# Kernel tuning notes

Hardware: AMD Instinct MI355X
Metric: run time of the kernel (lower is better)

## Reference

```python
import jax, jax.numpy as jnp
import numpy as np

N_NODES = 100000
N_EDGES = 800000
N_IN = 256
N_H = 128


def setup_inputs() -> dict:
    key = jax.random.key(0)
    ks = jax.random.split(key, 8)
    x_1 = jax.random.normal(ks[0], (1, N_NODES, N_IN), dtype=jnp.float32)
    x_2 = jax.random.normal(ks[1], (1, N_NODES, N_IN), dtype=jnp.float32)
    edge_index = jax.random.randint(ks[2], (2, N_EDGES), 0, N_NODES, dtype=jnp.int32)
    edge_weight = jax.random.uniform(ks[3], (N_EDGES,), dtype=jnp.float32)
    # xavier-uniform-ish init for fc weight (stored as [in, out])
    lim = float(np.sqrt(6.0 / (N_IN + N_H)))
    W_gcn = jax.random.uniform(ks[4], (N_IN, N_H), minval=-lim, maxval=lim, dtype=jnp.float32)
    gcn_bias = jnp.zeros((N_H,), dtype=jnp.float32)
    prelu_a = jnp.full((1,), 0.25, dtype=jnp.float32)  # PReLU default slope
    lim2 = float(np.sqrt(1.0 / N_H))
    lin_W = jax.random.uniform(ks[5], (N_H, N_H), minval=-lim2, maxval=lim2, dtype=jnp.float32)
    lin_b = jax.random.uniform(ks[6], (N_H,), minval=-lim2, maxval=lim2, dtype=jnp.float32)
    return {
        "x_1": x_1, "x_2": x_2, "edge_index": edge_index, "edge_weight": edge_weight,
        "W_gcn": W_gcn, "gcn_bias": gcn_bias, "prelu_a": prelu_a,
        "lin_W": lin_W, "lin_b": lin_b,
    }


def _prelu(x, a):
    return jnp.where(x >= 0, x, a * x)


def _gcn(feat, edge_index, edge_weight, W, b, a, n_nodes):
    # feat: [1, N, n_in] -> h: [N, n_h]
    h = jnp.squeeze(feat, 0) @ W
    row, col = edge_index[0], edge_index[1]
    # spmm: out[i] = sum_{e: row_e = i} w_e * h[col_e]
    msg = edge_weight[:, None] * h[col]            # [E, n_h]
    agg = jax.ops.segment_sum(msg, row, num_segments=n_nodes)  # [N, n_h]
    return _prelu(agg + b, a)                      # [N, n_h]


def reference(x_1, x_2, edge_index, edge_weight, W_gcn, gcn_bias, prelu_a, lin_W, lin_b):
    n = x_1.shape[1]
    h_1 = _gcn(x_1, edge_index, edge_weight, W_gcn, gcn_bias, prelu_a, n)
    h_2 = _gcn(x_2, edge_index, edge_weight, W_gcn, gcn_bias, prelu_a, n)
    z_1 = (h_1 @ lin_W + lin_b).sum(1)   # [N]
    z_2 = (h_2 @ lin_W + lin_b).sum(1)   # [N]
    return jnp.concatenate((z_1, z_2), 0)  # [2N]
```

## Files before the change

kernel.cpp:

```cpp
#include <hip/hip_runtime.h>

#define N_NODES 100000
#define N_EDGES 800000
#define N_IN    256
#define N_H     128
#define M_TOT   (2 * N_NODES)

typedef __bf16 bfx8 __attribute__((ext_vector_type(8)));
typedef unsigned short u16x8 __attribute__((ext_vector_type(8)));
typedef float fx4 __attribute__((ext_vector_type(4)));

__device__ inline unsigned short f2bf(float f) {
    union { float f; unsigned u; } v; v.f = f;
    return (unsigned short)((v.u + 0x7FFF + ((v.u >> 16) & 1)) >> 16);
}
__device__ inline float bf2f(unsigned short s) {
    union { unsigned u; float f; } v; v.u = ((unsigned)s) << 16;
    return v.f;
}

__device__ inline void async16(const void* g, void* l) {
    __builtin_amdgcn_global_load_lds((const __attribute__((address_space(1))) void*)g,
                                     (__attribute__((address_space(3))) void*)l, 16, 0, 0);
}

#define NSB2  3125
__global__ __launch_bounds__(256) void scatter_kernel(
        const int* __restrict__ ei, const float* __restrict__ ew,
        int* __restrict__ cursor, int2* __restrict__ edata) {
    int e = blockIdx.x * 256 + threadIdx.x;
    int row = ei[e];
    int pos = atomicAdd(cursor + row, 1);
    edata[pos] = make_int2(ei[N_EDGES + e] << 8, __float_as_int(ew[e]));
}

#define NT    12500
#define NTB1  6250
#define NGB3  1024

__global__ __launch_bounds__(256, 4) void gemm_kernel(
        const float* __restrict__ x1, const float* __restrict__ x2,
        const unsigned short* __restrict__ wT,
        unsigned short* __restrict__ hb) {
    __shared__ __align__(16) float Abuf[2][16][256];
    const int t = threadIdx.x;
    const int wv = t >> 6, ln = t & 63;
    const int quad = ln >> 4, l16 = ln & 15, sw = l16 & 7;

#define STAGE(buf, TT) do {                                                    \
        int br_ = (TT) >= NTB1;                                                \
        const float* xs_ = br_ ? x2 : x1;                                      \
        const float* base_ = xs_ + (size_t)((TT) - br_ * NTB1) * (16 * N_IN);  \
        _Pragma("unroll")                                                      \
        for (int i_ = 0; i_ < 4; ++i_) {                                       \
            int r_ = wv * 4 + i_;                                              \
            async16(base_ + (size_t)r_ * N_IN + ((ln ^ (r_ & 7)) << 2),        \
                    &Abuf[(buf)][r_][0]);                                      \
        }                                                                      \
    } while (0)

    int T = blockIdx.x;
    STAGE(0, T);

    bfx8 Bf[2][8];
#pragma unroll
    for (int c2 = 0; c2 < 2; ++c2)
#pragma unroll
        for (int kc = 0; kc < 8; ++kc)
            Bf[c2][kc] = *(const bfx8*)(wT +
                (size_t)(wv * 32 + c2 * 16 + l16) * N_IN + kc * 32 + quad * 8);
#pragma unroll
    for (int c2 = 0; c2 < 2; ++c2)
#pragma unroll
        for (int kc = 0; kc < 8; ++kc)
            asm volatile("" : "+v"(Bf[c2][kc]));

    int cur = 0;
    for (; T < NT; T += NGB3) {
        int Tn = T + NGB3;
        if (Tn < NT) {
            STAGE(cur ^ 1, Tn);
            asm volatile("s_waitcnt vmcnt(4)" ::: "memory");
        } else {
            asm volatile("s_waitcnt vmcnt(0)" ::: "memory");
        }
        asm volatile("s_barrier" ::: "memory");
        {
            int br = T >= NTB1;
            int node0 = (T - br * NTB1) * 16;
            fx4 acc0 = {0.f, 0.f, 0.f, 0.f}, acc1 = {0.f, 0.f, 0.f, 0.f};
            const float* rowp = &Abuf[cur][l16][0];
#pragma unroll
            for (int kc = 0; kc < 8; ++kc) {
                int s0 = kc * 8 + quad * 2;
                fx4 lo = *(const fx4*)(rowp + (((s0    ) ^ sw) << 2));
                fx4 hi = *(const fx4*)(rowp + (((s0 + 1) ^ sw) << 2));
                bfx8 af;
                af[0] = (__bf16)lo[0]; af[1] = (__bf16)lo[1];
                af[2] = (__bf16)lo[2]; af[3] = (__bf16)lo[3];
                af[4] = (__bf16)hi[0]; af[5] = (__bf16)hi[1];
                af[6] = (__bf16)hi[2]; af[7] = (__bf16)hi[3];
                acc0 = __builtin_amdgcn_mfma_f32_16x16x32_bf16(af, Bf[0][kc], acc0, 0, 0, 0);
                acc1 = __builtin_amdgcn_mfma_f32_16x16x32_bf16(af, Bf[1][kc], acc1, 0, 0, 0);
            }
            unsigned short* hp = hb + (size_t)node0 * 256 + br * 128 + wv * 32 + l16;
#pragma unroll
            for (int r = 0; r < 4; ++r) {
                size_t off = (size_t)(quad * 4 + r) * 256;
                hp[off]      = __builtin_bit_cast(unsigned short, (__bf16)acc0[r]);
                hp[off + 16] = __builtin_bit_cast(unsigned short, (__bf16)acc1[r]);
            }
        }
        asm volatile("s_barrier" ::: "memory");
        cur ^= 1;
    }
#undef STAGE
}

#define HIST_BLKS 3125
__global__ __launch_bounds__(256) void prep_kernel(const int* __restrict__ ei,
                                                   int* __restrict__ deg,
                                                   const float* __restrict__ W,
                                                   unsigned short* __restrict__ wT,
                                                   const float* __restrict__ linW,
                                                   const float* __restrict__ linb,
                                                   float* __restrict__ wsum) {
    const int t = threadIdx.x;
    if (blockIdx.x < HIST_BLKS) {
        int e = blockIdx.x * 256 + t;
        if (e < N_EDGES) atomicAdd(deg + ei[e], 1);
    } else if (blockIdx.x < HIST_BLKS + 32) {
        int kb = (blockIdx.x - HIST_BLKS) * 8;
#pragma unroll
        for (int p = 0; p < 4; ++p) {
            int idx = p * 256 + t;
            int k = kb + (idx >> 7), n = idx & 127;
            wT[(size_t)n * N_IN + k] = f2bf(W[(size_t)k * N_H + n]);
        }
    } else {
        int j = t;
        if (j < N_H) {
            float s = 0.f;
            for (int o = 0; o < N_H; ++o) s += linW[j * N_H + o];
            wsum[j] = s;
        }
        if (j == N_H) {
            float s = 0.f;
            for (int o = 0; o < N_H; ++o) s += linb[o];
            wsum[N_H] = s;
        }
    }
}

__global__ __launch_bounds__(256) void scan1_kernel(const int* __restrict__ deg,
                                                    int* __restrict__ part,
                                                    int* __restrict__ bsum) {
    __shared__ int s[256];
    int g = blockIdx.x * 256 + threadIdx.x;
    int v = (g < N_NODES) ? deg[g] : 0;
    s[threadIdx.x] = v;
    __syncthreads();
#pragma unroll
    for (int off = 1; off < 256; off <<= 1) {
        int t = (threadIdx.x >= off) ? s[threadIdx.x - off] : 0;
        __syncthreads();
        s[threadIdx.x] += t;
        __syncthreads();
    }
    if (g < N_NODES) part[g] = s[threadIdx.x] - v;
    if (threadIdx.x == 255) bsum[blockIdx.x] = s[255];
}

#define NBLK_SCAN 391
__global__ void scan2_kernel(int* __restrict__ bsum) {
    __shared__ int s[512];
    int v = (threadIdx.x < NBLK_SCAN) ? bsum[threadIdx.x] : 0;
    s[threadIdx.x] = v;
    __syncthreads();
#pragma unroll
    for (int off = 1; off < 512; off <<= 1) {
        int t = (threadIdx.x >= off) ? s[threadIdx.x - off] : 0;
        __syncthreads();
        s[threadIdx.x] += t;
        __syncthreads();
    }
    if (threadIdx.x < NBLK_SCAN) bsum[threadIdx.x] = s[threadIdx.x] - v;
}

__global__ __launch_bounds__(256) void scan3_kernel(const int* __restrict__ part,
                                                    const int* __restrict__ bsum,
                                                    int* __restrict__ off,
                                                    int* __restrict__ cursor) {
    int g = blockIdx.x * 256 + threadIdx.x;
    if (g < N_NODES) {
        int o = part[g] + bsum[blockIdx.x];
        off[g] = o;
        cursor[g] = o;
    }
    if (g == 0) off[N_NODES] = N_EDGES;
}

__global__ __launch_bounds__(256) void gcn_seg_kernel(const int* __restrict__ off,
                                                      const int2* __restrict__ edata,
                                                      const unsigned short* __restrict__ hb,
                                                      const float* __restrict__ gcn_bias,
                                                      const float* __restrict__ prelu_a,
                                                      const float* __restrict__ wsum,
                                                      float* __restrict__ zout) {
    const int wave = threadIdx.x >> 6, lane = threadIdx.x & 63;
    const int node = blockIdx.x * 4 + wave;
    const int s = __builtin_amdgcn_readfirstlane(off[node]);
    const int e = __builtin_amdgcn_readfirstlane(off[node + 1]);
    const int l2 = lane * 2;
    float a0 = 0.f, a1 = 0.f;
    float b0 = 0.f, b1 = 0.f;
    int i = s;
    for (; i + 1 < e; i += 2) {
        int2 E0 = edata[i], E1 = edata[i + 1];
        float w0 = __int_as_float(E0.y), w1 = __int_as_float(E1.y);
        ushort2 p10 = *(const ushort2*)(hb + E0.x + l2);
        ushort2 p20 = *(const ushort2*)(hb + E0.x + 128 + l2);
        ushort2 p11 = *(const ushort2*)(hb + E1.x + l2);
        ushort2 p21 = *(const ushort2*)(hb + E1.x + 128 + l2);
        a0 += w0 * bf2f(p10.x) + w1 * bf2f(p11.x);
        a1 += w0 * bf2f(p10.y) + w1 * bf2f(p11.y);
        b0 += w0 * bf2f(p20.x) + w1 * bf2f(p21.x);
        b1 += w0 * bf2f(p20.y) + w1 * bf2f(p21.y);
    }
    if (i < e) {
        int2 E0 = edata[i];
        float w0 = __int_as_float(E0.y);
        ushort2 p10 = *(const ushort2*)(hb + E0.x + l2);
        ushort2 p20 = *(const ushort2*)(hb + E0.x + 128 + l2);
        a0 += w0 * bf2f(p10.x);
        a1 += w0 * bf2f(p10.y);
        b0 += w0 * bf2f(p20.x);
        b1 += w0 * bf2f(p20.y);
    }
    const float alpha = prelu_a[0];
    const float g0 = gcn_bias[l2], g1 = gcn_bias[l2 + 1];
    const float q0 = wsum[l2],     q1 = wsum[l2 + 1];
    float v0 = a0 + g0, v1 = a1 + g1;
    float u0 = b0 + g0, u1 = b1 + g1;
    v0 = (v0 >= 0.f) ? v0 : alpha * v0;
    v1 = (v1 >= 0.f) ? v1 : alpha * v1;
    u0 = (u0 >= 0.f) ? u0 : alpha * u0;
    u1 = (u1 >= 0.f) ? u1 : alpha * u1;
    float s1 = v0 * q0 + v1 * q1;
    float s2 = u0 * q0 + u1 * q1;
#pragma unroll
    for (int o = 32; o; o >>= 1) {
        s1 += __shfl_down(s1, o, 64);
        s2 += __shfl_down(s2, o, 64);
    }
    if (lane == 0) {
        zout[node]           = s1 + wsum[128];
        zout[node + N_NODES] = s2 + wsum[128];
    }
}

extern "C" void kernel_launch(void* const* d_in, const int* in_sizes, int n_in,
                              void* d_out, int out_size, void* d_ws, size_t ws_size,
                              hipStream_t stream) {
    const float* x1 = (const float*)d_in[0];
    const float* x2 = (const float*)d_in[1];
    const int*   ei = (const int*)d_in[2];
    const float* ew = (const float*)d_in[3];
    const float* Wg = (const float*)d_in[4];
    const float* gb = (const float*)d_in[5];
    const float* pa = (const float*)d_in[6];
    const float* lW = (const float*)d_in[7];
    const float* lb = (const float*)d_in[8];
    float* zout = (float*)d_out;

    unsigned short* hb   = (unsigned short*)d_ws;
    int2*  edata  = (int2*)(hb + (size_t)M_TOT * N_H);
    unsigned short* wT   = (unsigned short*)(edata + N_EDGES);
    int*   deg    = (int*)(wT + N_IN * N_H);
    int*   part   = deg + 100096;
    int*   off    = part + 100096;
    int*   cursor = off + 100096;
    int*   bsum   = cursor + 100096;
    float* wsum   = (float*)(bsum + 512);

    hipMemsetAsync(deg, 0, (size_t)N_NODES * sizeof(int), stream);
    prep_kernel<<<HIST_BLKS + 33, 256, 0, stream>>>(ei, deg, Wg, wT, lW, lb, wsum);
    scan1_kernel<<<NBLK_SCAN, 256, 0, stream>>>(deg, part, bsum);
    scan2_kernel<<<1, 512, 0, stream>>>(bsum);
    scan3_kernel<<<NBLK_SCAN, 256, 0, stream>>>(part, bsum, off, cursor);
    scatter_kernel<<<NSB2, 256, 0, stream>>>(ei, ew, cursor, edata);
    gemm_kernel<<<NGB3, 256, 0, stream>>>(x1, x2, wT, hb);
    gcn_seg_kernel<<<N_NODES / 4, 256, 0, stream>>>(off, edata, hb, gb, pa, wsum, zout);
}
```

Baseline: 393.0 us.

## Fuse edge scatter into GEMM launch, drop persistent loop, unroll gather by four

Scatter and GEMM are merged into one launch: the first blocks do the edge scatter and the rest each compute one 16-row tile, replacing the persistent double-buffered GEMM loop. This removes a kernel boundary and lets the scatter overlap the GEMM. The lin_W row-sum in prep is reworked as a parallel wave reduction instead of a serial per-thread loop, and the gather loop in gcn_seg is unrolled to four edges per iteration for more loads in flight. The trade-off is that each GEMM block now reloads the B fragments and loses cross-tile prefetch overlap, with many more short-lived blocks.

```diff
diff --git a/kernel.cpp b/kernel.cpp
--- a/kernel.cpp
+++ b/kernel.cpp
@@ -24,43 +24,38 @@
                                      (__attribute__((address_space(3))) void*)l, 16, 0, 0);
 }
 
-#define NSB2  3125
-__global__ __launch_bounds__(256) void scatter_kernel(
+#define NTB1  6250
+#define NSB   3125
+#define NGB   12500
+
+__global__ __launch_bounds__(256, 4) void gemm_scatter_kernel(
+        const float* __restrict__ x1, const float* __restrict__ x2,
+        const unsigned short* __restrict__ wT,
+        unsigned short* __restrict__ hb,
         const int* __restrict__ ei, const float* __restrict__ ew,
         int* __restrict__ cursor, int2* __restrict__ edata) {
-    int e = blockIdx.x * 256 + threadIdx.x;
-    int row = ei[e];
-    int pos = atomicAdd(cursor + row, 1);
-    edata[pos] = make_int2(ei[N_EDGES + e] << 8, __float_as_int(ew[e]));
-}
-
-#define NT    12500
-#define NTB1  6250
-#define NGB3  1024
-
-__global__ __launch_bounds__(256, 4) void gemm_kernel(
-        const float* __restrict__ x1, const float* __restrict__ x2,
-        const unsigned short* __restrict__ wT,
-        unsigned short* __restrict__ hb) {
-    __shared__ __align__(16) float Abuf[2][16][256];
     const int t = threadIdx.x;
+    if (blockIdx.x < NSB) {
+        int e = blockIdx.x * 256 + t;
+        int row = ei[e];
+        int pos = atomicAdd(cursor + row, 1);
+        edata[pos] = make_int2(ei[N_EDGES + e] << 8, __float_as_int(ew[e]));
+        return;
+    }
+    __shared__ __align__(16) float Abuf[16][256];
+    const int T = blockIdx.x - NSB;
     const int wv = t >> 6, ln = t & 63;
     const int quad = ln >> 4, l16 = ln & 15, sw = l16 & 7;
-
-#define STAGE(buf, TT) do {                                                    \
-        int br_ = (TT) >= NTB1;                                                \
-        const float* xs_ = br_ ? x2 : x1;                                      \
-        const float* base_ = xs_ + (size_t)((TT) - br_ * NTB1) * (16 * N_IN);  \
-        _Pragma("unroll")                                                      \
-        for (int i_ = 0; i_ < 4; ++i_) {                                       \
-            int r_ = wv * 4 + i_;                                              \
-            async16(base_ + (size_t)r_ * N_IN + ((ln ^ (r_ & 7)) << 2),        \
-                    &Abuf[(buf)][r_][0]);                                      \
-        }                                                                      \
-    } while (0)
-
-    int T = blockIdx.x;
-    STAGE(0, T);
+    const int br = T >= NTB1;
+    const float* xs = br ? x2 : x1;
+    const int node0 = (T - br * NTB1) * 16;
+    const float* base = xs + (size_t)node0 * N_IN;
+
+#pragma unroll
+    for (int i = 0; i < 4; ++i) {
+        int r = wv * 4 + i;
+        async16(base + (size_t)r * N_IN + ((ln ^ (r & 7)) << 2), &Abuf[r][0]);
+    }
 
     bfx8 Bf[2][8];
 #pragma unroll
@@ -69,52 +64,31 @@
         for (int kc = 0; kc < 8; ++kc)
             Bf[c2][kc] = *(const bfx8*)(wT +
                 (size_t)(wv * 32 + c2 * 16 + l16) * N_IN + kc * 32 + quad * 8);
-#pragma unroll
-    for (int c2 = 0; c2 < 2; ++c2)
-#pragma unroll
-        for (int kc = 0; kc < 8; ++kc)
-            asm volatile("" : "+v"(Bf[c2][kc]));
-
-    int cur = 0;
-    for (; T < NT; T += NGB3) {
-        int Tn = T + NGB3;
-        if (Tn < NT) {
-            STAGE(cur ^ 1, Tn);
-            asm volatile("s_waitcnt vmcnt(4)" ::: "memory");
-        } else {
-            asm volatile("s_waitcnt vmcnt(0)" ::: "memory");
-        }
-        asm volatile("s_barrier" ::: "memory");
-        {
-            int br = T >= NTB1;
-            int node0 = (T - br * NTB1) * 16;
-            fx4 acc0 = {0.f, 0.f, 0.f, 0.f}, acc1 = {0.f, 0.f, 0.f, 0.f};
-            const float* rowp = &Abuf[cur][l16][0];
-#pragma unroll
-            for (int kc = 0; kc < 8; ++kc) {
-                int s0 = kc * 8 + quad * 2;
-                fx4 lo = *(const fx4*)(rowp + (((s0    ) ^ sw) << 2));
-                fx4 hi = *(const fx4*)(rowp + (((s0 + 1) ^ sw) << 2));
-                bfx8 af;
-                af[0] = (__bf16)lo[0]; af[1] = (__bf16)lo[1];
-                af[2] = (__bf16)lo[2]; af[3] = (__bf16)lo[3];
-                af[4] = (__bf16)hi[0]; af[5] = (__bf16)hi[1];
-                af[6] = (__bf16)hi[2]; af[7] = (__bf16)hi[3];
-                acc0 = __builtin_amdgcn_mfma_f32_16x16x32_bf16(af, Bf[0][kc], acc0, 0, 0, 0);
-                acc1 = __builtin_amdgcn_mfma_f32_16x16x32_bf16(af, Bf[1][kc], acc1, 0, 0, 0);
-            }
-            unsigned short* hp = hb + (size_t)node0 * 256 + br * 128 + wv * 32 + l16;
-#pragma unroll
-            for (int r = 0; r < 4; ++r) {
-                size_t off = (size_t)(quad * 4 + r) * 256;
-                hp[off]      = __builtin_bit_cast(unsigned short, (__bf16)acc0[r]);
-                hp[off + 16] = __builtin_bit_cast(unsigned short, (__bf16)acc1[r]);
-            }
-        }
-        asm volatile("s_barrier" ::: "memory");
-        cur ^= 1;
-    }
-#undef STAGE
+
+    __syncthreads();
+
+    fx4 acc0 = {0.f, 0.f, 0.f, 0.f}, acc1 = {0.f, 0.f, 0.f, 0.f};
+    const float* rowp = &Abuf[l16][0];
+#pragma unroll
+    for (int kc = 0; kc < 8; ++kc) {
+        int s0 = kc * 8 + quad * 2;
+        fx4 lo = *(const fx4*)(rowp + (((s0    ) ^ sw) << 2));
+        fx4 hi = *(const fx4*)(rowp + (((s0 + 1) ^ sw) << 2));
+        bfx8 af;
+        af[0] = (__bf16)lo[0]; af[1] = (__bf16)lo[1];
+        af[2] = (__bf16)lo[2]; af[3] = (__bf16)lo[3];
+        af[4] = (__bf16)hi[0]; af[5] = (__bf16)hi[1];
+        af[6] = (__bf16)hi[2]; af[7] = (__bf16)hi[3];
+        acc0 = __builtin_amdgcn_mfma_f32_16x16x32_bf16(af, Bf[0][kc], acc0, 0, 0, 0);
+        acc1 = __builtin_amdgcn_mfma_f32_16x16x32_bf16(af, Bf[1][kc], acc1, 0, 0, 0);
+    }
+    unsigned short* hp = hb + (size_t)node0 * 256 + br * 128 + wv * 32 + l16;
+#pragma unroll
+    for (int r = 0; r < 4; ++r) {
+        size_t off = (size_t)(quad * 4 + r) * 256;
+        hp[off]      = __builtin_bit_cast(unsigned short, (__bf16)acc0[r]);
+        hp[off + 16] = __builtin_bit_cast(unsigned short, (__bf16)acc1[r]);
+    }
 }
 
 #define HIST_BLKS 3125
@@ -138,16 +112,23 @@
             wT[(size_t)n * N_IN + k] = f2bf(W[(size_t)k * N_H + n]);
         }
     } else {
-        int j = t;
-        if (j < N_H) {
-            float s = 0.f;
-            for (int o = 0; o < N_H; ++o) s += linW[j * N_H + o];
-            wsum[j] = s;
+        __shared__ float part[N_H];
+        if (t < N_H) part[t] = 0.f;
+        __syncthreads();
+        const int wvp = t >> 6, lnp = t & 63;
+        for (int ii = 0; ii < 64; ++ii) {
+            float v = linW[ii * 256 + t];
+#pragma unroll
+            for (int o = 32; o; o >>= 1) v += __shfl_down(v, o, 64);
+            if (lnp == 0) atomicAdd(&part[2 * ii + (wvp >> 1)], v);
         }
-        if (j == N_H) {
-            float s = 0.f;
-            for (int o = 0; o < N_H; ++o) s += linb[o];
-            wsum[N_H] = s;
+        __syncthreads();
+        if (t < N_H) wsum[t] = part[t];
+        if (wvp == 2) {
+            float v = linb[lnp] + linb[lnp + 64];
+#pragma unroll
+            for (int o = 32; o; o >>= 1) v += __shfl_down(v, o, 64);
+            if (lnp == 0) wsum[N_H] = v;
         }
     }
 }
@@ -215,19 +196,25 @@
     float a0 = 0.f, a1 = 0.f;
     float b0 = 0.f, b1 = 0.f;
     int i = s;
-    for (; i + 1 < e; i += 2) {
+    for (; i + 3 < e; i += 4) {
         int2 E0 = edata[i], E1 = edata[i + 1];
+        int2 E2 = edata[i + 2], E3 = edata[i + 3];
         float w0 = __int_as_float(E0.y), w1 = __int_as_float(E1.y);
+        float w2 = __int_as_float(E2.y), w3 = __int_as_float(E3.y);
         ushort2 p10 = *(const ushort2*)(hb + E0.x + l2);
         ushort2 p20 = *(const ushort2*)(hb + E0.x + 128 + l2);
         ushort2 p11 = *(const ushort2*)(hb + E1.x + l2);
         ushort2 p21 = *(const ushort2*)(hb + E1.x + 128 + l2);
-        a0 += w0 * bf2f(p10.x) + w1 * bf2f(p11.x);
-        a1 += w0 * bf2f(p10.y) + w1 * bf2f(p11.y);
-        b0 += w0 * bf2f(p20.x) + w1 * bf2f(p21.x);
-        b1 += w0 * bf2f(p20.y) + w1 * bf2f(p21.y);
-    }
-    if (i < e) {
+        ushort2 p12 = *(const ushort2*)(hb + E2.x + l2);
+        ushort2 p22 = *(const ushort2*)(hb + E2.x + 128 + l2);
+        ushort2 p13 = *(const ushort2*)(hb + E3.x + l2);
+        ushort2 p23 = *(const ushort2*)(hb + E3.x + 128 + l2);
+        a0 += w0 * bf2f(p10.x) + w1 * bf2f(p11.x) + w2 * bf2f(p12.x) + w3 * bf2f(p13.x);
+        a1 += w0 * bf2f(p10.y) + w1 * bf2f(p11.y) + w2 * bf2f(p12.y) + w3 * bf2f(p13.y);
+        b0 += w0 * bf2f(p20.x) + w1 * bf2f(p21.x) + w2 * bf2f(p22.x) + w3 * bf2f(p23.x);
+        b1 += w0 * bf2f(p20.y) + w1 * bf2f(p21.y) + w2 * bf2f(p22.y) + w3 * bf2f(p23.y);
+    }
+    for (; i < e; ++i) {
         int2 E0 = edata[i];
         float w0 = __int_as_float(E0.y);
         ushort2 p10 = *(const ushort2*)(hb + E0.x + l2);
@@ -288,7 +275,7 @@
     scan1_kernel<<<NBLK_SCAN, 256, 0, stream>>>(deg, part, bsum);
     scan2_kernel<<<1, 512, 0, stream>>>(bsum);
     scan3_kernel<<<NBLK_SCAN, 256, 0, stream>>>(part, bsum, off, cursor);
-    scatter_kernel<<<NSB2, 256, 0, stream>>>(ei, ew, cursor, edata);
-    gemm_kernel<<<NGB3, 256, 0, stream>>>(x1, x2, wT, hb);
+    gemm_scatter_kernel<<<NSB + NGB, 256, 0, stream>>>(x1, x2, wT, hb,
+                                                       ei, ew, cursor, edata);
     gcn_seg_kernel<<<N_NODES / 4, 256, 0, stream>>>(off, edata, hb, gb, pa, wsum, zout);
 }
```

Result: slower. 457.7 us (+16.5%).
